# Kernel tuning notes

Measured on AMD Instinct MI355X. Metric: run time of the kernel, lower is better.

## Reference

```python
import jax, jax.numpy as jnp
import numpy as np

S, E, CAP = 4096, 64, 128


def setup_inputs() -> dict:
    key = jax.random.key(0)
    k1, k2 = jax.random.split(key)
    logits = jax.random.normal(k1, (S, E), dtype=jnp.float32)
    noise = jax.random.normal(k2, (S, E), dtype=jnp.float32)
    return {"logits": logits, "noise": noise, "capacity": CAP}


def reference(logits, noise, capacity):
    # logits, noise: [S, E]; capacity: python int
    gates = jax.nn.softmax(logits, axis=1)                      # [S, E]
    num_experts = gates.shape[1]

    # top-1 expert
    indices1_s = jnp.argmax(gates, axis=1)                      # [S]
    mask1 = jax.nn.one_hot(indices1_s, num_experts, dtype=jnp.int32)

    # top-2 expert from noised logits with top-1 masked out
    logits_w_noise = logits + noise
    neg_min = jnp.finfo(logits.dtype).min
    logits_except1 = jnp.where(mask1 > 0, neg_min, logits_w_noise)
    indices2_s = jnp.argmax(logits_except1, axis=1)
    mask2 = jax.nn.one_hot(indices2_s, num_experts, dtype=jnp.int32)

    # capacity locations (running count per expert over tokens)
    locations1 = jnp.cumsum(mask1, axis=0) - 1                  # [S, E]
    locations2 = jnp.cumsum(mask2, axis=0) - 1
    locations2 = locations2 + jnp.sum(mask1, axis=0, keepdims=True)

    # load-balancing aux loss
    me = jnp.mean(gates, axis=0)
    ce = jnp.mean(mask1.astype(logits.dtype), axis=0)
    l_aux = jnp.mean(me * ce) * num_experts * num_experts

    # drop tokens over capacity
    mask1 = mask1 * (locations1 < capacity).astype(mask1.dtype)
    mask2 = mask2 * (locations2 < capacity).astype(mask2.dtype)

    locations1_s = jnp.sum(locations1 * mask1, axis=1)          # [S]
    locations2_s = jnp.sum(locations2 * mask2, axis=1)

    mask1_f = mask1.astype(logits.dtype)
    mask2_f = mask2.astype(logits.dtype)
    gates1_s = jnp.einsum('se,se->s', gates, mask1_f)
    gates2_s = jnp.einsum('se,se->s', gates, mask2_f)
    denom_s = jnp.maximum(gates1_s + gates2_s, jnp.finfo(logits.dtype).eps)
    gates1_s = gates1_s / denom_s
    gates2_s = gates2_s / denom_s

    gates1 = gates1_s[:, None] * mask1_f                        # [S, E]
    gates2 = gates2_s[:, None] * mask2_f

    locations1_sc = jax.nn.one_hot(locations1_s, capacity, dtype=logits.dtype)
    locations2_sc = jax.nn.one_hot(locations2_s, capacity, dtype=logits.dtype)

    combine_weights = (gates1[:, :, None] * locations1_sc[:, None, :]
                       + gates2[:, :, None] * locations2_sc[:, None, :])  # [S, E, C]
    dispatch_mask = combine_weights.astype(bool)
    return l_aux, combine_weights, dispatch_mask
```

## Files before the change

### kernel.cpp

```cpp
#include <hip/hip_runtime.h>
#include <float.h>
#include <math.h>

#define SS 4096
#define EE 64
#define CAPC 128
#define ROW (EE * CAPC)
#define SEC (4096LL * 64 * 128)

__global__ __launch_bounds__(256) void gate_kernel(const float* __restrict__ logits,
                                                   const float* __restrict__ noise,
                                                   int* __restrict__ idx1s,
                                                   int* __restrict__ idx2s,
                                                   float* __restrict__ g1raw,
                                                   float* __restrict__ g2raw,
                                                   float* __restrict__ partial) {
    const int tid  = threadIdx.x;
    const int wave = tid >> 6;
    const int lane = tid & 63;
    const int s    = blockIdx.x * 4 + wave;

    const float l = logits[s * EE + lane];
    const float n = noise[s * EE + lane];

    float v = l; int bi = lane;
    #pragma unroll
    for (int off = 32; off; off >>= 1) {
        float v2 = __shfl_xor(v, off, 64);
        int   i2 = __shfl_xor(bi, off, 64);
        if (v2 > v || (v2 == v && i2 < bi)) { v = v2; bi = i2; }
    }
    const int idx1 = bi;
    const float m = v;

    float e = expf(l - m);
    float sum = e;
    #pragma unroll
    for (int off = 32; off; off >>= 1) sum += __shfl_xor(sum, off, 64);
    const float gate = e / sum;
    const float g1 = __shfl(gate, idx1, 64);

    float lw = (lane == idx1) ? -FLT_MAX : (l + n);
    float v2v = lw; int bi2 = lane;
    #pragma unroll
    for (int off = 32; off; off >>= 1) {
        float v2 = __shfl_xor(v2v, off, 64);
        int   i2 = __shfl_xor(bi2, off, 64);
        if (v2 > v2v || (v2 == v2v && i2 < bi2)) { v2v = v2; bi2 = i2; }
    }
    const int idx2 = bi2;
    const float g2 = __shfl(gate, idx2, 64);

    if (lane == 0) {
        idx1s[s] = idx1;
        idx2s[s] = idx2;
        g1raw[s] = g1;
        g2raw[s] = g2;
    }

    __shared__ float sg[256];
    sg[tid] = gate;
    __syncthreads();
    if (tid < 64) {
        partial[blockIdx.x * 64 + tid] =
            sg[tid] + sg[tid + 64] + sg[tid + 128] + sg[tid + 192];
    }
}

__global__ __launch_bounds__(64) void rank_kernel(const int* __restrict__ idx1s,
                                                  const int* __restrict__ idx2s,
                                                  int* __restrict__ wrank1,
                                                  int* __restrict__ wrank2,
                                                  int* __restrict__ cnt1,
                                                  int* __restrict__ cnt2,
                                                  const float* __restrict__ partial,
                                                  float* __restrict__ partial2) {
    __shared__ int li1[64], li2[64];
    const int t = threadIdx.x;
    const int chunk = blockIdx.x;
    const int s = chunk * 64 + t;
    li1[t] = idx1s[s];
    li2[t] = idx2s[s];

    float acc = 0.f;
    #pragma unroll
    for (int k = 0; k < 16; ++k) acc += partial[(chunk * 16 + k) * 64 + t];
    partial2[chunk * 64 + t] = acc;

    __syncthreads();
    const int my1 = li1[t], my2 = li2[t];
    int r1 = 0, r2 = 0, c1 = 0, c2 = 0;
    #pragma unroll 8
    for (int j = 0; j < 64; ++j) {
        const int a = li1[j], b = li2[j];
        r1 += (int)((j < t) & (a == my1));
        r2 += (int)((j < t) & (b == my2));
        c1 += (int)(a == t);
        c2 += (int)(b == t);
    }
    wrank1[s] = r1;
    wrank2[s] = r2;
    cnt1[chunk * 64 + t] = c1;
    cnt2[chunk * 64 + t] = c2;
}

__global__ __launch_bounds__(64) void scan_kernel(const int* __restrict__ cnt1,
                                                  const int* __restrict__ cnt2,
                                                  int* __restrict__ off1,
                                                  int* __restrict__ off2,
                                                  int* __restrict__ count1,
                                                  const float* __restrict__ partial2,
                                                  float* __restrict__ laux_ws) {
    const int e = threadIdx.x;
    int o1 = 0, o2 = 0;
    #pragma unroll 8
    for (int c = 0; c < 64; ++c) {
        off1[c * 64 + e] = o1; o1 += cnt1[c * 64 + e];
        off2[c * 64 + e] = o2; o2 += cnt2[c * 64 + e];
    }
    count1[e] = o1;

    float gs = 0.f;
    #pragma unroll 8
    for (int c = 0; c < 64; ++c) gs += partial2[c * 64 + e];

    float prod = gs * (float)o1;
    #pragma unroll
    for (int off = 32; off; off >>= 1) prod += __shfl_xor(prod, off, 64);
    if (e == 0) {
        laux_ws[0] = prod * (float)EE / ((float)SS * (float)SS);
    }
}

__global__ __launch_bounds__(256) void zero_scatter_kernel(const int* __restrict__ idx1s,
                                                           const int* __restrict__ idx2s,
                                                           const int* __restrict__ wrank1,
                                                           const int* __restrict__ wrank2,
                                                           const int* __restrict__ off1,
                                                           const int* __restrict__ off2,
                                                           const int* __restrict__ count1,
                                                           const float* __restrict__ g1raw,
                                                           const float* __restrict__ g2raw,
                                                           const float* __restrict__ laux_ws,
                                                           float* __restrict__ out) {
    const int tid = threadIdx.x;
    const int t0  = blockIdx.x * 4;
    const long cb = (long)t0 * ROW;

    int i1 = 0, i2 = 0, loc1 = 0, loc2 = 0;
    float g1 = 0.f, g2 = 0.f;
    bool k1 = false, k2 = false;
    if (tid < 4) {
        const int s = t0 + tid;
        i1 = idx1s[s];
        i2 = idx2s[s];
        const int chunk = s >> 6;
        loc1 = wrank1[s] + off1[chunk * 64 + i1];
        loc2 = wrank2[s] + off2[chunk * 64 + i2] + count1[i2];
        g1 = g1raw[s];
        g2 = g2raw[s];
        k1 = loc1 < CAPC;
        k2 = loc2 < CAPC;
        g1 = k1 ? g1 : 0.f;
        g2 = k2 ? g2 : 0.f;
        const float denom = fmaxf(g1 + g2, 1.1920929e-07f);
        g1 /= denom;
        g2 /= denom;
    }

    const float4 z = make_float4(0.f, 0.f, 0.f, 0.f);
    float4* p4 = (float4*)(out + cb + 4);
    float4* q4 = (float4*)(out + SEC + cb + 4);
    #pragma unroll
    for (int i = tid; i < 8191; i += 256) p4[i] = z;
    #pragma unroll
    for (int i = tid; i < 8191; i += 256) q4[i] = z;
    if (tid < 3) {
        out[cb + 1 + tid] = 0.f;
        out[SEC + cb + 1 + tid] = 0.f;
    } else if (tid == 3) {
        out[cb + 4L * ROW] = 0.f;
        out[SEC + cb + 4L * ROW] = 0.f;
    }
    __syncthreads();

    if (tid < 4) {
        const int s = t0 + tid;
        float* combine = out + 1;
        float* mask    = out + 1 + SEC;
        const long base = (long)s * ROW;
        if (k1 && g1 != 0.f) {
            const long p = base + (long)i1 * CAPC + loc1;
            combine[p] = g1;
            mask[p]    = 1.f;
        }
        if (k2 && g2 != 0.f) {
            const long p = base + (long)i2 * CAPC + loc2;
            combine[p] = g2;
            mask[p]    = 1.f;
        }
    }
    if (tid == 4 && blockIdx.x == 0) {
        out[0] = laux_ws[0];
    }
}

extern "C" void kernel_launch(void* const* d_in, const int* in_sizes, int n_in,
                              void* d_out, int out_size, void* d_ws, size_t ws_size,
                              hipStream_t stream) {
    const float* logits = (const float*)d_in[0];
    const float* noise  = (const float*)d_in[1];
    float* out = (float*)d_out;

    char* ws = (char*)d_ws;
    int*   idx1s    = (int*)  (ws + 0);
    int*   idx2s    = (int*)  (ws + 16384);
    int*   wrank1   = (int*)  (ws + 32768);
    int*   wrank2   = (int*)  (ws + 49152);
    float* g1raw    = (float*)(ws + 65536);
    float* g2raw    = (float*)(ws + 81920);
    int*   cnt1     = (int*)  (ws + 98304);
    int*   cnt2     = (int*)  (ws + 114688);
    int*   off1     = (int*)  (ws + 131072);
    int*   off2     = (int*)  (ws + 147456);
    int*   count1   = (int*)  (ws + 163840);
    float* laux_ws  = (float*)(ws + 164352);
    float* partial  = (float*)(ws + 196608);
    float* partial2 = (float*)(ws + 458752);

    gate_kernel<<<SS / 4, 256, 0, stream>>>(logits, noise, idx1s, idx2s, g1raw, g2raw, partial);
    rank_kernel<<<64, 64, 0, stream>>>(idx1s, idx2s, wrank1, wrank2, cnt1, cnt2, partial, partial2);
    scan_kernel<<<1, 64, 0, stream>>>(cnt1, cnt2, off1, off2, count1, partial2, laux_ws);
    zero_scatter_kernel<<<SS / 4, 256, 0, stream>>>(idx1s, idx2s, wrank1, wrank2,
                                                    off1, off2, count1, g1raw, g2raw,
                                                    laux_ws, out);
}
```

Before: 284.9 us.

## Fuse gating, ranking, scan and scatter into one cooperative kernel

Replaces the four-kernel pipeline with a single cooperative kernel of 256 blocks × 1024 threads, each block handling 16 tokens. Per-block expert counts and in-block ranks are kept in shared memory. Grid-wide syncs replace the kernel boundaries, and the serial prefix scan over block counts runs in block 0. The zeroing of the large combine and mask output is overlapped with the gating work before the first grid sync. This removes launch overheads and intermediate global round-trips, in exchange for grid.sync costs, a serial 256-step scan in one block, and one wave of 256 blocks having to write the whole ~268MB output.

```diff
diff --git a/kernel.cpp b/kernel.cpp
--- a/kernel.cpp
+++ b/kernel.cpp
@@ -1,27 +1,46 @@
 #include <hip/hip_runtime.h>
+#include <hip/hip_cooperative_groups.h>
 #include <float.h>
 #include <math.h>
+
+namespace cg = cooperative_groups;
 
 #define SS 4096
 #define EE 64
 #define CAPC 128
-#define ROW (EE * CAPC)
+#define ROW 8192
 #define SEC (4096LL * 64 * 128)
-
-__global__ __launch_bounds__(256) void gate_kernel(const float* __restrict__ logits,
-                                                   const float* __restrict__ noise,
-                                                   int* __restrict__ idx1s,
-                                                   int* __restrict__ idx2s,
-                                                   float* __restrict__ g1raw,
-                                                   float* __restrict__ g2raw,
-                                                   float* __restrict__ partial) {
+#define NBLK 256
+#define TPB 1024
+#define TPB_TOK 16
+
+__global__ __launch_bounds__(1024) void fused_kernel(
+    const float* __restrict__ logits,
+    const float* __restrict__ noise,
+    int*   __restrict__ bc1,
+    int*   __restrict__ bc2,
+    int*   __restrict__ boff1,
+    int*   __restrict__ boff2,
+    int*   __restrict__ count1,
+    float* __restrict__ pg,
+    float* __restrict__ out)
+{
+    cg::grid_group grid = cg::this_grid();
     const int tid  = threadIdx.x;
     const int wave = tid >> 6;
     const int lane = tid & 63;
-    const int s    = blockIdx.x * 4 + wave;
-
+    const int b    = blockIdx.x;
+
+    __shared__ int   s_idx1[TPB_TOK], s_idx2[TPB_TOK];
+    __shared__ int   s_lr1[TPB_TOK],  s_lr2[TPB_TOK];
+    __shared__ float s_g1[TPB_TOK],   s_g2[TPB_TOK];
+    __shared__ float s_gate[TPB_TOK][64];
+    __shared__ float s_red[16][64];
+    __shared__ float s_laux;
+
+    const int s = b * TPB_TOK + wave;
     const float l = logits[s * EE + lane];
-    const float n = noise[s * EE + lane];
+    const float n = noise [s * EE + lane];
 
     float v = l; int bi = lane;
     #pragma unroll
@@ -31,164 +50,127 @@
         if (v2 > v || (v2 == v && i2 < bi)) { v = v2; bi = i2; }
     }
     const int idx1 = bi;
-    const float m = v;
-
-    float e = expf(l - m);
+
+    float e = expf(l - v);
     float sum = e;
     #pragma unroll
     for (int off = 32; off; off >>= 1) sum += __shfl_xor(sum, off, 64);
     const float gate = e / sum;
-    const float g1 = __shfl(gate, idx1, 64);
 
     float lw = (lane == idx1) ? -FLT_MAX : (l + n);
     float v2v = lw; int bi2 = lane;
     #pragma unroll
     for (int off = 32; off; off >>= 1) {
-        float v2 = __shfl_xor(v2v, off, 64);
+        float q  = __shfl_xor(v2v, off, 64);
         int   i2 = __shfl_xor(bi2, off, 64);
-        if (v2 > v2v || (v2 == v2v && i2 < bi2)) { v2v = v2; bi2 = i2; }
+        if (q > v2v || (q == v2v && i2 < bi2)) { v2v = q; bi2 = i2; }
     }
     const int idx2 = bi2;
-    const float g2 = __shfl(gate, idx2, 64);
-
+
+    s_gate[wave][lane] = gate;
+    const float g1v = __shfl(gate, idx1, 64);
+    const float g2v = __shfl(gate, idx2, 64);
     if (lane == 0) {
-        idx1s[s] = idx1;
-        idx2s[s] = idx2;
-        g1raw[s] = g1;
-        g2raw[s] = g2;
-    }
-
-    __shared__ float sg[256];
-    sg[tid] = gate;
+        s_idx1[wave] = idx1;
+        s_idx2[wave] = idx2;
+        s_g1[wave] = g1v;
+        s_g2[wave] = g2v;
+    }
     __syncthreads();
+
     if (tid < 64) {
-        partial[blockIdx.x * 64 + tid] =
-            sg[tid] + sg[tid + 64] + sg[tid + 128] + sg[tid + 192];
-    }
-}
-
-__global__ __launch_bounds__(64) void rank_kernel(const int* __restrict__ idx1s,
-                                                  const int* __restrict__ idx2s,
-                                                  int* __restrict__ wrank1,
-                                                  int* __restrict__ wrank2,
-                                                  int* __restrict__ cnt1,
-                                                  int* __restrict__ cnt2,
-                                                  const float* __restrict__ partial,
-                                                  float* __restrict__ partial2) {
-    __shared__ int li1[64], li2[64];
-    const int t = threadIdx.x;
-    const int chunk = blockIdx.x;
-    const int s = chunk * 64 + t;
-    li1[t] = idx1s[s];
-    li2[t] = idx2s[s];
-
-    float acc = 0.f;
-    #pragma unroll
-    for (int k = 0; k < 16; ++k) acc += partial[(chunk * 16 + k) * 64 + t];
-    partial2[chunk * 64 + t] = acc;
-
-    __syncthreads();
-    const int my1 = li1[t], my2 = li2[t];
-    int r1 = 0, r2 = 0, c1 = 0, c2 = 0;
-    #pragma unroll 8
-    for (int j = 0; j < 64; ++j) {
-        const int a = li1[j], b = li2[j];
-        r1 += (int)((j < t) & (a == my1));
-        r2 += (int)((j < t) & (b == my2));
-        c1 += (int)(a == t);
-        c2 += (int)(b == t);
-    }
-    wrank1[s] = r1;
-    wrank2[s] = r2;
-    cnt1[chunk * 64 + t] = c1;
-    cnt2[chunk * 64 + t] = c2;
-}
-
-__global__ __launch_bounds__(64) void scan_kernel(const int* __restrict__ cnt1,
-                                                  const int* __restrict__ cnt2,
-                                                  int* __restrict__ off1,
-                                                  int* __restrict__ off2,
-                                                  int* __restrict__ count1,
-                                                  const float* __restrict__ partial2,
-                                                  float* __restrict__ laux_ws) {
-    const int e = threadIdx.x;
-    int o1 = 0, o2 = 0;
-    #pragma unroll 8
-    for (int c = 0; c < 64; ++c) {
-        off1[c * 64 + e] = o1; o1 += cnt1[c * 64 + e];
-        off2[c * 64 + e] = o2; o2 += cnt2[c * 64 + e];
-    }
-    count1[e] = o1;
-
-    float gs = 0.f;
-    #pragma unroll 8
-    for (int c = 0; c < 64; ++c) gs += partial2[c * 64 + e];
-
-    float prod = gs * (float)o1;
-    #pragma unroll
-    for (int off = 32; off; off >>= 1) prod += __shfl_xor(prod, off, 64);
-    if (e == 0) {
-        laux_ws[0] = prod * (float)EE / ((float)SS * (float)SS);
-    }
-}
-
-__global__ __launch_bounds__(256) void zero_scatter_kernel(const int* __restrict__ idx1s,
-                                                           const int* __restrict__ idx2s,
-                                                           const int* __restrict__ wrank1,
-                                                           const int* __restrict__ wrank2,
-                                                           const int* __restrict__ off1,
-                                                           const int* __restrict__ off2,
-                                                           const int* __restrict__ count1,
-                                                           const float* __restrict__ g1raw,
-                                                           const float* __restrict__ g2raw,
-                                                           const float* __restrict__ laux_ws,
-                                                           float* __restrict__ out) {
-    const int tid = threadIdx.x;
-    const int t0  = blockIdx.x * 4;
-    const long cb = (long)t0 * ROW;
-
-    int i1 = 0, i2 = 0, loc1 = 0, loc2 = 0;
-    float g1 = 0.f, g2 = 0.f;
-    bool k1 = false, k2 = false;
-    if (tid < 4) {
-        const int s = t0 + tid;
-        i1 = idx1s[s];
-        i2 = idx2s[s];
-        const int chunk = s >> 6;
-        loc1 = wrank1[s] + off1[chunk * 64 + i1];
-        loc2 = wrank2[s] + off2[chunk * 64 + i2] + count1[i2];
-        g1 = g1raw[s];
-        g2 = g2raw[s];
-        k1 = loc1 < CAPC;
-        k2 = loc2 < CAPC;
+        int c1 = 0, c2 = 0;
+        float gs = 0.f;
+        #pragma unroll
+        for (int j = 0; j < TPB_TOK; ++j) {
+            c1 += (s_idx1[j] == tid);
+            c2 += (s_idx2[j] == tid);
+            gs += s_gate[j][tid];
+        }
+        bc1[b * 64 + tid] = c1;
+        bc2[b * 64 + tid] = c2;
+        pg [b * 64 + tid] = gs;
+    } else if (tid < 64 + TPB_TOK) {
+        const int t = tid - 64;
+        const int m1 = s_idx1[t], m2 = s_idx2[t];
+        int r1 = 0, r2 = 0;
+        for (int j = 0; j < t; ++j) {
+            r1 += (s_idx1[j] == m1);
+            r2 += (s_idx2[j] == m2);
+        }
+        s_lr1[t] = r1;
+        s_lr2[t] = r2;
+    }
+
+    {
+        const long cb = (long)b * (TPB_TOK * ROW);
+        float4* p4 = (float4*)(out + cb + 4);
+        float4* q4 = (float4*)(out + SEC + cb + 4);
+        const float4 z = make_float4(0.f, 0.f, 0.f, 0.f);
+        for (int i = tid; i < 32767; i += TPB) p4[i] = z;
+        for (int i = tid; i < 32767; i += TPB) q4[i] = z;
+        if (tid < 3) {
+            out[cb + 1 + tid] = 0.f;
+            out[SEC + cb + 1 + tid] = 0.f;
+        } else if (tid == 3) {
+            out[cb + (long)TPB_TOK * ROW] = 0.f;
+            out[SEC + cb + (long)TPB_TOK * ROW] = 0.f;
+        }
+    }
+
+    grid.sync();
+
+    if (b == 0) {
+        {
+            const int e = tid & 63, g = tid >> 6;
+            float acc = 0.f;
+            #pragma unroll
+            for (int k = 0; k < 16; ++k) acc += pg[(g * 16 + k) * 64 + e];
+            s_red[g][e] = acc;
+        }
+        __syncthreads();
+        if (tid < 64) {
+            int o1 = 0;
+            for (int blk = 0; blk < NBLK; ++blk) {
+                boff1[blk * 64 + tid] = o1;
+                o1 += bc1[blk * 64 + tid];
+            }
+            count1[tid] = o1;
+            float gs = 0.f;
+            #pragma unroll
+            for (int g = 0; g < 16; ++g) gs += s_red[g][tid];
+            float prod = gs * (float)o1;
+            #pragma unroll
+            for (int off = 32; off; off >>= 1) prod += __shfl_xor(prod, off, 64);
+            if (tid == 0)
+                s_laux = prod * (float)EE / ((float)SS * (float)SS);
+        } else if (tid < 128) {
+            const int e2 = tid - 64;
+            int o2 = 0;
+            for (int blk = 0; blk < NBLK; ++blk) {
+                boff2[blk * 64 + e2] = o2;
+                o2 += bc2[blk * 64 + e2];
+            }
+        }
+    }
+
+    grid.sync();
+
+    if (tid < TPB_TOK) {
+        const int t  = tid;
+        const int i1 = s_idx1[t], i2 = s_idx2[t];
+        const int loc1 = s_lr1[t] + boff1[b * 64 + i1];
+        const int loc2 = s_lr2[t] + boff2[b * 64 + i2] + count1[i2];
+        float g1 = s_g1[t], g2 = s_g2[t];
+        const bool k1 = loc1 < CAPC, k2 = loc2 < CAPC;
         g1 = k1 ? g1 : 0.f;
         g2 = k2 ? g2 : 0.f;
         const float denom = fmaxf(g1 + g2, 1.1920929e-07f);
         g1 /= denom;
         g2 /= denom;
-    }
-
-    const float4 z = make_float4(0.f, 0.f, 0.f, 0.f);
-    float4* p4 = (float4*)(out + cb + 4);
-    float4* q4 = (float4*)(out + SEC + cb + 4);
-    #pragma unroll
-    for (int i = tid; i < 8191; i += 256) p4[i] = z;
-    #pragma unroll
-    for (int i = tid; i < 8191; i += 256) q4[i] = z;
-    if (tid < 3) {
-        out[cb + 1 + tid] = 0.f;
-        out[SEC + cb + 1 + tid] = 0.f;
-    } else if (tid == 3) {
-        out[cb + 4L * ROW] = 0.f;
-        out[SEC + cb + 4L * ROW] = 0.f;
-    }
-    __syncthreads();
-
-    if (tid < 4) {
-        const int s = t0 + tid;
         float* combine = out + 1;
         float* mask    = out + 1 + SEC;
-        const long base = (long)s * ROW;
+        const long base = (long)(b * TPB_TOK + t) * ROW;
         if (k1 && g1 != 0.f) {
             const long p = base + (long)i1 * CAPC + loc1;
             combine[p] = g1;
@@ -199,9 +181,8 @@
             combine[p] = g2;
             mask[p]    = 1.f;
         }
-    }
-    if (tid == 4 && blockIdx.x == 0) {
-        out[0] = laux_ws[0];
+    } else if (tid == TPB_TOK && b == 0) {
+        out[0] = s_laux;
     }
 }
 
@@ -213,25 +194,16 @@
     float* out = (float*)d_out;
 
     char* ws = (char*)d_ws;
-    int*   idx1s    = (int*)  (ws + 0);
-    int*   idx2s    = (int*)  (ws + 16384);
-    int*   wrank1   = (int*)  (ws + 32768);
-    int*   wrank2   = (int*)  (ws + 49152);
-    float* g1raw    = (float*)(ws + 65536);
-    float* g2raw    = (float*)(ws + 81920);
-    int*   cnt1     = (int*)  (ws + 98304);
-    int*   cnt2     = (int*)  (ws + 114688);
-    int*   off1     = (int*)  (ws + 131072);
-    int*   off2     = (int*)  (ws + 147456);
-    int*   count1   = (int*)  (ws + 163840);
-    float* laux_ws  = (float*)(ws + 164352);
-    float* partial  = (float*)(ws + 196608);
-    float* partial2 = (float*)(ws + 458752);
-
-    gate_kernel<<<SS / 4, 256, 0, stream>>>(logits, noise, idx1s, idx2s, g1raw, g2raw, partial);
-    rank_kernel<<<64, 64, 0, stream>>>(idx1s, idx2s, wrank1, wrank2, cnt1, cnt2, partial, partial2);
-    scan_kernel<<<1, 64, 0, stream>>>(cnt1, cnt2, off1, off2, count1, partial2, laux_ws);
-    zero_scatter_kernel<<<SS / 4, 256, 0, stream>>>(idx1s, idx2s, wrank1, wrank2,
-                                                    off1, off2, count1, g1raw, g2raw,
-                                                    laux_ws, out);
+    int*   bc1    = (int*)  (ws + 0);
+    int*   bc2    = (int*)  (ws + 65536);
+    int*   boff1  = (int*)  (ws + 131072);
+    int*   boff2  = (int*)  (ws + 196608);
+    int*   count1 = (int*)  (ws + 262144);
+    float* pg     = (float*)(ws + 266240);
+
+    void* args[] = {(void*)&logits, (void*)&noise, (void*)&bc1, (void*)&bc2,
+                    (void*)&boff1, (void*)&boff2, (void*)&count1, (void*)&pg,
+                    (void*)&out};
+    hipLaunchCooperativeKernel((const void*)fused_kernel, dim3(NBLK), dim3(TPB),
+                               args, 0, stream);
 }
```

Result: slower. 371.7 us (+30.4%).
